# Kernel optimization log

Hardware: AMD Instinct MI355X
Metric: run time of the kernel (lower is better)

The kernel has to match this reference:

```python
import jax, jax.numpy as jnp
import numpy as np

HIDDEN = 2048
NH = 32        # query heads
NKV = 4        # kv heads
D = 128        # head dim
T = 2048       # tokens
WINDOW = 512   # sliding window
EPS = 1e-6
THETA = 1000000.0
SCALE = D ** -0.5


def setup_inputs() -> dict:
    key = jax.random.key(0)
    k1, k2, k3 = jax.random.split(key, 3)
    return {
        "positions": jnp.arange(T, dtype=jnp.int64) if jax.config.jax_enable_x64 else jnp.arange(T, dtype=jnp.int32),
        "hidden_states": jax.random.normal(k1, (T, HIDDEN), dtype=jnp.float32),
        "w_qkv": jax.random.normal(k2, (HIDDEN, (NH + 2 * NKV) * D), dtype=jnp.float32) * 0.02,
        "w_o": jax.random.normal(k3, (NH * D, HIDDEN), dtype=jnp.float32) * 0.02,
        "q_norm_w": jnp.ones((D,), dtype=jnp.float32),
        "k_norm_w": jnp.ones((D,), dtype=jnp.float32),
    }


def _rms_norm(x, w):
    # x: [..., D]; per-head RMSNorm
    var = jnp.mean(x * x, axis=-1, keepdims=True)
    return x * jax.lax.rsqrt(var + EPS) * w


def _rope(x, positions):
    # x: [T, H, D], neox-style rotary over full head dim
    inv_freq = 1.0 / (THETA ** (jnp.arange(0, D, 2, dtype=jnp.float32) / D))  # [D/2]
    freqs = positions.astype(jnp.float32)[:, None] * inv_freq                 # [T, D/2]
    cos = jnp.cos(freqs)[:, None, :]
    sin = jnp.sin(freqs)[:, None, :]
    x1, x2 = x[..., : D // 2], x[..., D // 2 :]
    return jnp.concatenate([x1 * cos - x2 * sin, x2 * cos + x1 * sin], axis=-1)


def reference(positions, hidden_states, w_qkv, w_o, q_norm_w, k_norm_w):
    qkv = hidden_states @ w_qkv                                   # [T, (NH+2NKV)*D]
    q, k, v = jnp.split(qkv, [NH * D, (NH + NKV) * D], axis=-1)
    q = _rms_norm(q.reshape(T, NH, D), q_norm_w)
    k = _rms_norm(k.reshape(T, NKV, D), k_norm_w)
    v = v.reshape(T, NKV, D)
    q = _rope(q, positions)
    k = _rope(k, positions)
    # GQA: expand kv heads to query heads
    rep = NH // NKV
    k = jnp.repeat(k, rep, axis=1)                                # [T, NH, D]
    v = jnp.repeat(v, rep, axis=1)
    scores = jnp.einsum("qhd,khd->hqk", q, k) * SCALE             # [NH, T, T]
    i = jnp.arange(T)[:, None]
    j = jnp.arange(T)[None, :]
    mask = (j <= i) & (i - j < WINDOW)                            # causal sliding window
    scores = jnp.where(mask[None, :, :], scores, jnp.finfo(scores.dtype).min)
    probs = jax.nn.softmax(scores, axis=-1)
    out = jnp.einsum("hqk,khd->qhd", probs, v).reshape(T, NH * D)
    return out @ w_o
```

## Files before the change

### kernel.cpp

```cpp
#include <hip/hip_runtime.h>
#include <math.h>

#define T      2048
#define HIDDEN 2048
#define NH     32
#define NKV    4
#define D      128
#define WINDOW 512
#define QKVW   ((NH + 2 * NKV) * D)
#define ODIM   (NH * D)
#define EPS    1e-6f
#define SCALE  0.08838834764831845f
#define PSTR   68
#define ESTR   136
#define VSTR   36
#define QMUL   ((float)(0.08838834764831845 * 1.4426950408889634))
#define MLOG2E 5.7707801635558536f

typedef _Float16 f16x8 __attribute__((ext_vector_type(8)));
typedef _Float16 f16x4 __attribute__((ext_vector_type(4)));
typedef float    f32x4 __attribute__((ext_vector_type(4)));


__device__ __forceinline__ void gl2lds16(const void* g, void* l) {
  __builtin_amdgcn_global_load_lds((const __attribute__((address_space(1))) void*)g,
                                   (__attribute__((address_space(3))) void*)l,
                                   16, 0, 0);
}

#define NB_A  2048
#define NB_B1 2560
#define NB_B2 2048

__device__ __forceinline__ void pack_b_region(const float* __restrict__ W,
                                              _Float16* __restrict__ Bp,
                                              int N, int kt, int ng, int tid,
                                              _Float16* __restrict__ LS) {
  const int r = tid >> 3;
  const int c0 = (tid & 7) * 16;
  const float* src = W + (size_t)(kt * 32 + r) * N + ng * 128 + c0;
#pragma unroll
  for (int v = 0; v < 4; ++v) {
    const float4 f = *(const float4*)(src + v * 4);
    LS[r * 132 + c0 + v * 4 + 0] = (_Float16)f.x;
    LS[r * 132 + c0 + v * 4 + 1] = (_Float16)f.y;
    LS[r * 132 + c0 + v * 4 + 2] = (_Float16)f.z;
    LS[r * 132 + c0 + v * 4 + 3] = (_Float16)f.w;
  }
  __syncthreads();
#pragma unroll
  for (int i = 0; i < 2; ++i) {
    const int ch = tid * 2 + i;
    const int tile = ch >> 6;
    const int cc = ch & 63;
    const int q = cc >> 4, o = cc & 15;
    f16x8 v;
#pragma unroll
    for (int j = 0; j < 8; ++j) v[j] = LS[(q * 8 + j) * 132 + tile * 16 + o];
    *(f16x8*)(Bp + ((size_t)(kt * (N / 16) + ng * 8 + tile) * 512) + cc * 8) = v;
  }
}

__global__ __launch_bounds__(256)
void prep(const float* __restrict__ hidden, const float* __restrict__ w_qkv,
          const float* __restrict__ w_o, const int* __restrict__ positions,
          _Float16* __restrict__ Ah1, _Float16* __restrict__ Bp1,
          _Float16* __restrict__ Bp2, float* __restrict__ cosT,
          float* __restrict__ sinT) {
  __shared__ _Float16 LS[32 * 132];
  const int bx = blockIdx.x;
  const int tid = threadIdx.x;
  if (bx < NB_A) {
    const int cid = bx * 256 + tid;
    const int c = cid & 63;
    const int tile = cid >> 6;
    const int mtg = tile & (T / 16 - 1);
    const int kt = tile >> 7;
    const float* src = hidden + (size_t)(mtg * 16 + (c & 15)) * HIDDEN + kt * 32 + (c >> 4) * 8;
    const float4 a = *(const float4*)src;
    const float4 b = *(const float4*)(src + 4);
    f16x8 h;
    h[0] = (_Float16)a.x; h[1] = (_Float16)a.y; h[2] = (_Float16)a.z; h[3] = (_Float16)a.w;
    h[4] = (_Float16)b.x; h[5] = (_Float16)b.y; h[6] = (_Float16)b.z; h[7] = (_Float16)b.w;
    *(f16x8*)(Ah1 + (size_t)cid * 8) = h;
  } else if (bx < NB_A + NB_B1) {
    const int idx = bx - NB_A;
    pack_b_region(w_qkv, Bp1, QKVW, idx / 40, idx % 40, tid, LS);
  } else if (bx < NB_A + NB_B1 + NB_B2) {
    const int idx = bx - NB_A - NB_B1;
    pack_b_region(w_o, Bp2, HIDDEN, idx / 16, idx % 16, tid, LS);
  } else {
    const int p0 = (bx - NB_A - NB_B1 - NB_B2) * 64 + (tid >> 6) * 16;
    const int j = tid & 63;
    const float invf = (float)pow(1.0e6, -(double)j / 64.0);
#pragma unroll 4
    for (int i = 0; i < 16; ++i) {
      const int t = p0 + i;
      const float ang = (float)positions[t] * invf;
      cosT[t * 64 + j] = cosf(ang);
      sinT[t * 64 + j] = sinf(ang);
    }
  }
}

#define KSTEPS 64

__global__ __launch_bounds__(256, 3)
void gemm_qkv(const _Float16* __restrict__ Apk, const _Float16* __restrict__ Bpk,
              const float* __restrict__ qnw, const float* __restrict__ knw,
              const float* __restrict__ cosT, const float* __restrict__ sinT,
              _Float16* __restrict__ Qpk, _Float16* __restrict__ Kpk,
              _Float16* __restrict__ Vpk) {
  extern __shared__ _Float16 SM[];
  const int tid = threadIdx.x;
  const int lane = tid & 63;
  const int wv = tid >> 6;
  const int l15 = lane & 15;
  const int l4 = lane >> 4;
  const int bx = blockIdx.x, by = blockIdx.y;

  f32x4 acc[2][8];
#pragma unroll
  for (int i = 0; i < 2; ++i)
#pragma unroll
    for (int j = 0; j < 8; ++j) acc[i][j] = (f32x4)0.f;

  auto stage = [&](int k, int s) {
    const int u = wv * 4 + s;
    char* dst = (char*)SM + (k % 3) * 16384 +
                (u < 8 ? u * 1024 : 8192 + (u - 8) * 1024);
    const char* src = (u < 8)
        ? (const char*)Apk + ((size_t)k * (T / 16) + by * 8 + u) * 1024 + lane * 16
        : (const char*)Bpk + ((size_t)k * (QKVW / 16) + bx * 8 + (u - 8)) * 1024 + lane * 16;
    gl2lds16(src, dst);
  };

#pragma unroll
  for (int k = 0; k < 2; ++k)
#pragma unroll
    for (int s = 0; s < 4; ++s) stage(k, s);
  asm volatile("s_waitcnt vmcnt(4)" ::: "memory");
  __builtin_amdgcn_s_barrier();
  __builtin_amdgcn_sched_barrier(0);

  int slot = 0;
  for (int t = 0; t < KSTEPS; ++t) {
    const _Float16* As = SM + slot * 8192;
    const _Float16* Bs = As + 4096;
    f16x8 af[2], bf[8];
#pragma unroll
    for (int i = 0; i < 2; ++i)
      af[i] = *(const f16x8*)(As + (wv * 2 + i) * 512 + lane * 8);
#pragma unroll
    for (int j = 0; j < 8; ++j)
      bf[j] = *(const f16x8*)(Bs + j * 512 + lane * 8);
    if (t + 2 < KSTEPS)
#pragma unroll
      for (int s = 0; s < 4; ++s) stage(t + 2, s);
    __builtin_amdgcn_s_setprio(1);
#pragma unroll
    for (int i = 0; i < 2; ++i)
#pragma unroll
      for (int j = 0; j < 8; ++j)
        acc[i][j] = __builtin_amdgcn_mfma_f32_16x16x32_f16(af[i], bf[j], acc[i][j], 0, 0, 0);
    __builtin_amdgcn_s_setprio(0);
    if (t < KSTEPS - 2)       asm volatile("s_waitcnt vmcnt(4)" ::: "memory");
    else if (t == KSTEPS - 2) asm volatile("s_waitcnt vmcnt(0)" ::: "memory");
    __builtin_amdgcn_s_barrier();
    __builtin_amdgcn_sched_barrier(0);
    slot = (slot == 2) ? 0 : slot + 1;
  }
  __syncthreads();

  if (bx < NH + NKV) {
    const bool isq = bx < NH;
    const float* w = isq ? qnw : knw;
    const float omul = isq ? QMUL : 1.0f;
    float wcol[8];
#pragma unroll
    for (int j = 0; j < 8; ++j) wcol[j] = w[j * 16 + l15];

    _Float16* ex = SM + wv * (32 * ESTR);
#pragma unroll
    for (int i = 0; i < 2; ++i)
#pragma unroll
      for (int r = 0; r < 4; ++r) {
        float ss = 0.f;
#pragma unroll
        for (int j = 0; j < 8; ++j) ss += acc[i][j][r] * acc[i][j][r];
        ss += __shfl_xor(ss, 1); ss += __shfl_xor(ss, 2);
        ss += __shfl_xor(ss, 4); ss += __shfl_xor(ss, 8);
        const float rn = 1.0f / sqrtf(ss * (1.0f / D) + EPS);
        const int row = i * 16 + l4 * 4 + r;
        const int t = by * 128 + wv * 32 + row;
#pragma unroll
        for (int j = 0; j < 4; ++j) {
          const int jc = j * 16 + l15;
          const float c = cosT[t * 64 + jc];
          const float s = sinT[t * 64 + jc];
          const float x1 = acc[i][j][r] * rn * wcol[j];
          const float x2 = acc[i][j + 4][r] * rn * wcol[j + 4];
          ex[row * ESTR + jc]      = (_Float16)((x1 * c - x2 * s) * omul);
          ex[row * ESTR + 64 + jc] = (_Float16)((x2 * c + x1 * s) * omul);
        }
      }
    const int hl = isq ? bx : bx - NH;
    _Float16* dst0 = isq ? Qpk : Kpk;
#pragma unroll
    for (int u = 0; u < 2; ++u) {
      const int qt = by * 8 + wv * 2 + u;
#pragma unroll
      for (int ds = 0; ds < 4; ++ds) {
        const f16x8 frag = *(const f16x8*)(ex + (u * 16 + l15) * ESTR + ds * 32 + l4 * 8);
        *(f16x8*)(dst0 + ((size_t)(hl * 128 + qt) * 4 + ds) * 512 + lane * 8) = frag;
      }
    }
  } else {
    const int kvh = bx - NH - NKV;
    _Float16* exv = SM + wv * (128 * VSTR);
#pragma unroll
    for (int i = 0; i < 2; ++i)
#pragma unroll
      for (int j = 0; j < 8; ++j) {
        f16x4 v4;
#pragma unroll
        for (int r = 0; r < 4; ++r) v4[r] = (_Float16)acc[i][j][r];
        *(f16x4*)(exv + (j * 16 + l15) * VSTR + i * 16 + l4 * 4) = v4;
      }
    const int kt64 = by * 2 + (wv >> 1);
    const int ks = wv & 1;
#pragma unroll
    for (int dt = 0; dt < 8; ++dt) {
      const f16x4 lo = *(const f16x4*)(exv + (dt * 16 + l15) * VSTR + l4 * 8);
      const f16x4 hi = *(const f16x4*)(exv + (dt * 16 + l15) * VSTR + l4 * 8 + 4);
      f16x8 h8;
#pragma unroll
      for (int r = 0; r < 4; ++r) { h8[r] = lo[r]; h8[r + 4] = hi[r]; }
      *(f16x8*)(Vpk + (((size_t)(kvh * 32 + kt64) * 2 + ks) * 8 + dt) * 512 + lane * 8) = h8;
    }
  }
}

__global__ __launch_bounds__(256, 3)
void gemm_f16p(const _Float16* __restrict__ Apk, const _Float16* __restrict__ Bpk,
               float* __restrict__ C0, float* __restrict__ C1,
               int M, int N, int nkt) {
  extern __shared__ _Float16 SM[];
  const int tid = threadIdx.x;
  const int lane = tid & 63;
  const int wv = tid >> 6;
  const int wr = wv & 1, wc = wv >> 1;
  const int kt0 = blockIdx.z * nkt;
  float* __restrict__ C = blockIdx.z ? C1 : C0;

  f32x4 acc[4][4];
#pragma unroll
  for (int i = 0; i < 4; ++i)
#pragma unroll
    for (int j = 0; j < 4; ++j) acc[i][j] = (f32x4)0.f;

  const size_t Astep = (size_t)(M >> 4) * 1024;
  const size_t Bstep = (size_t)(N >> 4) * 1024;
  const char* Ag = (const char*)Apk + (size_t)kt0 * Astep +
                   (size_t)(blockIdx.y * 8) * 1024 + lane * 16;
  const char* Bg = (const char*)Bpk + (size_t)kt0 * Bstep +
                   (size_t)(blockIdx.x * 8) * 1024 + lane * 16;

  auto stage = [&](int k, int s) {
    const int u = wv * 4 + s;
    char* dst = (char*)SM + (k % 3) * 16384 +
                (u < 8 ? u * 1024 : 8192 + (u - 8) * 1024);
    const char* src = (u < 8) ? Ag + (size_t)k * Astep + u * 1024
                              : Bg + (size_t)k * Bstep + (u - 8) * 1024;
    gl2lds16(src, dst);
  };

#pragma unroll
  for (int k = 0; k < 2; ++k)
#pragma unroll
    for (int s = 0; s < 4; ++s) stage(k, s);
  asm volatile("s_waitcnt vmcnt(4)" ::: "memory");
  __builtin_amdgcn_s_barrier();
  __builtin_amdgcn_sched_barrier(0);

  int slot = 0;
  for (int t = 0; t < nkt; ++t) {
    const _Float16* As = SM + slot * 8192;
    const _Float16* Bs = As + 4096;
    f16x8 af[4], bf[4];
#pragma unroll
    for (int i = 0; i < 4; ++i)
      af[i] = *(const f16x8*)(As + (wr * 4 + i) * 512 + lane * 8);
#pragma unroll
    for (int j = 0; j < 4; ++j)
      bf[j] = *(const f16x8*)(Bs + (wc * 4 + j) * 512 + lane * 8);
    if (t + 2 < nkt)
#pragma unroll
      for (int s = 0; s < 4; ++s) stage(t + 2, s);
    __builtin_amdgcn_s_setprio(1);
#pragma unroll
    for (int i = 0; i < 4; ++i)
#pragma unroll
      for (int j = 0; j < 4; ++j)
        acc[i][j] = __builtin_amdgcn_mfma_f32_16x16x32_f16(af[i], bf[j], acc[i][j], 0, 0, 0);
    __builtin_amdgcn_s_setprio(0);
    if (t < nkt - 2)       asm volatile("s_waitcnt vmcnt(4)" ::: "memory");
    else if (t == nkt - 2) asm volatile("s_waitcnt vmcnt(0)" ::: "memory");
    __builtin_amdgcn_s_barrier();
    __builtin_amdgcn_sched_barrier(0);
    slot = (slot == 2) ? 0 : slot + 1;
  }

  const int row0 = blockIdx.y * 128 + wr * 64 + ((lane >> 4) << 2);
  const int col0 = blockIdx.x * 128 + wc * 64 + (lane & 15);
#pragma unroll
  for (int i = 0; i < 4; ++i)
#pragma unroll
    for (int j = 0; j < 4; ++j) {
#pragma unroll
      for (int r = 0; r < 4; ++r)
        C[(size_t)(row0 + i * 16 + r) * N + col0 + j * 16] = acc[i][j][r];
    }
}

__global__ __launch_bounds__(256)
void reduce_add(const float4* __restrict__ a, const float4* __restrict__ b,
                float4* __restrict__ o, int n4) {
  for (int i = blockIdx.x * 256 + threadIdx.x; i < n4; i += gridDim.x * 256) {
    const float4 x = a[i], y = b[i];
    o[i] = make_float4(x.x + y.x, x.y + y.y, x.z + y.z, x.w + y.w);
  }
}

__global__ __launch_bounds__(256)
void attn_mfma(const _Float16* __restrict__ Qpk, const _Float16* __restrict__ Kpk,
               const _Float16* __restrict__ Vpk, _Float16* __restrict__ Ap2) {
  const int h = blockIdx.x;
  const int q0 = blockIdx.y * 128;
  const int kvh = h >> 3;
  const int tid = threadIdx.x;
  const int lane = tid & 63;
  const int wv = tid >> 6;
  const int l15 = lane & 15;
  const int l4 = lane >> 4;

  __shared__ _Float16 SM[8192 + 2 * 8192 + 4 * 32 * PSTR];
  _Float16* Ks = SM;
  _Float16* Vs = SM + 8192;
  _Float16* Pw = SM + 24576 + wv * 32 * PSTR;

  f16x8 qfA[4], qfB[4];
  {
    const _Float16* qa = Qpk + ((size_t)h * 128 + (q0 >> 4) + wv * 2) * 2048 + lane * 8;
#pragma unroll
    for (int ds = 0; ds < 4; ++ds) {
      qfA[ds] = *(const f16x8*)(qa + ds * 512);
      qfB[ds] = *(const f16x8*)(qa + 2048 + ds * 512);
    }
  }

  f16x8 ones;
#pragma unroll
  for (int j = 0; j < 8; ++j) ones[j] = (_Float16)1.0f;

  f32x4 OA[8], OB[8];
#pragma unroll
  for (int dt = 0; dt < 8; ++dt) { OA[dt] = (f32x4)0.f; OB[dt] = (f32x4)0.f; }
  f32x4 LA = (f32x4)0.f, LB = (f32x4)0.f;

  int kstart = q0 - (WINDOW - 1);
  if (kstart < 0) kstart = 0;
  kstart &= ~63;
  const int kend = q0 + 128;

  auto stageKV = [&](int kt2, int vb) {
    const _Float16* Kg = Kpk + ((size_t)kvh * 128 + (kt2 >> 4)) * 2048 + lane * 8;
    const _Float16* Vg = Vpk + ((size_t)kvh * 32 + (kt2 >> 6)) * 8192 + lane * 8;
#pragma unroll
    for (int t = wv; t < 16; t += 4) {
      gl2lds16(Kg + t * 512, (char*)Ks + t * 1024);
      gl2lds16(Vg + t * 512, (char*)(Vs + vb * 8192) + t * 1024);
    }
  };

  stageKV(kstart, 0);
  asm volatile("s_waitcnt vmcnt(0)" ::: "memory");
  __builtin_amdgcn_s_barrier();
  __builtin_amdgcn_sched_barrier(0);

  int vbuf = 0;
  for (int kt = kstart; kt < kend; kt += 64) {
    f32x4 sA[4], sB[4];
#pragma unroll
    for (int nt = 0; nt < 4; ++nt) { sA[nt] = (f32x4)(-MLOG2E); sB[nt] = (f32x4)(-MLOG2E); }
    __builtin_amdgcn_s_setprio(1);
#pragma unroll
    for (int ds = 0; ds < 4; ++ds) {
#pragma unroll
      for (int nt = 0; nt < 4; ++nt) {
        const f16x8 kf = *(const f16x8*)(Ks + (nt * 4 + ds) * 512 + lane * 8);
        sA[nt] = __builtin_amdgcn_mfma_f32_16x16x32_f16(qfA[ds], kf, sA[nt], 0, 0, 0);
        sB[nt] = __builtin_amdgcn_mfma_f32_16x16x32_f16(qfB[ds], kf, sB[nt], 0, 0, 0);
      }
    }
    __builtin_amdgcn_s_setprio(0);
    __builtin_amdgcn_s_barrier();
    __builtin_amdgcn_sched_barrier(0);
    if (kt + 64 < kend) stageKV(kt + 64, vbuf ^ 1);

    const int qbA = q0 + wv * 32 + l4 * 4;
    const int kb = kt + l15;
#pragma unroll
    for (int nt = 0; nt < 4; ++nt) {
      const int kidx = kb + nt * 16;
#pragma unroll
      for (int r = 0; r < 4; ++r) {
        float pA = __builtin_amdgcn_exp2f(sA[nt][r]);
        float pB = __builtin_amdgcn_exp2f(sB[nt][r]);
        pA = ((unsigned)(qbA + r - kidx) < WINDOW) ? pA : 0.f;
        pB = ((unsigned)(qbA + 16 + r - kidx) < WINDOW) ? pB : 0.f;
        Pw[(l4 * 4 + r) * PSTR + nt * 16 + l15] = (_Float16)pA;
        Pw[(16 + l4 * 4 + r) * PSTR + nt * 16 + l15] = (_Float16)pB;
      }
    }

    const _Float16* Vcur = Vs + vbuf * 8192;
    __builtin_amdgcn_s_setprio(1);
#pragma unroll
    for (int ks = 0; ks < 2; ++ks) {
      const f16x8 pfA = *(const f16x8*)(Pw + l15 * PSTR + ks * 32 + l4 * 8);
      const f16x8 pfB = *(const f16x8*)(Pw + (16 + l15) * PSTR + ks * 32 + l4 * 8);
      LA = __builtin_amdgcn_mfma_f32_16x16x32_f16(pfA, ones, LA, 0, 0, 0);
      LB = __builtin_amdgcn_mfma_f32_16x16x32_f16(pfB, ones, LB, 0, 0, 0);
#pragma unroll
      for (int dt = 0; dt < 8; ++dt) {
        const f16x8 vf = *(const f16x8*)(Vcur + (ks * 8 + dt) * 512 + lane * 8);
        OA[dt] = __builtin_amdgcn_mfma_f32_16x16x32_f16(pfA, vf, OA[dt], 0, 0, 0);
        OB[dt] = __builtin_amdgcn_mfma_f32_16x16x32_f16(pfB, vf, OB[dt], 0, 0, 0);
      }
    }
    __builtin_amdgcn_s_setprio(0);
    asm volatile("s_waitcnt vmcnt(0)" ::: "memory");
    __builtin_amdgcn_s_barrier();
    __builtin_amdgcn_sched_barrier(0);
    vbuf ^= 1;
  }

  _Float16* Tw = SM + wv * 16 * ESTR;
#pragma unroll
  for (int half = 0; half < 2; ++half) {
    const f32x4* O = half ? OB : OA;
    const f32x4  L = half ? LB : LA;
    float inv[4];
#pragma unroll
    for (int r = 0; r < 4; ++r) inv[r] = 1.0f / L[r];
#pragma unroll
    for (int dt = 0; dt < 8; ++dt)
#pragma unroll
      for (int r = 0; r < 4; ++r)
        Tw[(l4 * 4 + r) * ESTR + dt * 16 + l15] = (_Float16)(O[dt][r] * inv[r]);
    const int qt = (q0 >> 4) + wv * 2 + half;
#pragma unroll
    for (int ds = 0; ds < 4; ++ds) {
      const f16x8 frag = *(const f16x8*)(Tw + l15 * ESTR + ds * 32 + l4 * 8);
      *(f16x8*)(Ap2 + ((size_t)(h * 4 + ds) * 128 + qt) * 512 + lane * 8) = frag;
    }
  }
}

extern "C" void kernel_launch(void* const* d_in, const int* in_sizes, int n_in,
                              void* d_out, int out_size, void* d_ws, size_t ws_size,
                              hipStream_t stream) {
  const int*   positions = (const int*)d_in[0];
  const float* hidden    = (const float*)d_in[1];
  const float* w_qkv     = (const float*)d_in[2];
  const float* w_o       = (const float*)d_in[3];
  const float* q_norm_w  = (const float*)d_in[4];
  const float* k_norm_w  = (const float*)d_in[5];
  float* out = (float*)d_out;

  char* ws = (char*)d_ws;
  _Float16* Kpk = (_Float16*)ws;
  _Float16* Vpk = Kpk + (size_t)T * NKV * D;
  ws += (size_t)T * QKVW * 4;
  _Float16* Ap2 = (_Float16*)ws;
  float* P0 = (float*)(ws + (size_t)T * ODIM * 2);
  ws += (size_t)T * ODIM * 4;
  float* cosT = (float*)ws;  ws += (size_t)T * 64 * 4;
  float* sinT = (float*)ws;  ws += (size_t)T * 64 * 4;
  _Float16* Bp1 = (_Float16*)ws; ws += (size_t)HIDDEN * QKVW * 2;
  _Float16* Bp2 = (_Float16*)ws; ws += (size_t)ODIM * HIDDEN * 2;
  _Float16* Ah1 = (_Float16*)ws; ws += (size_t)T * HIDDEN * 2;
  _Float16* Qpk = (_Float16*)ws;
  float* P1 = (float*)Qpk;
  ws += (size_t)T * ODIM * 2;

  prep<<<dim3(NB_A + NB_B1 + NB_B2 + T / 64), 256, 0, stream>>>(
      hidden, w_qkv, w_o, positions, Ah1, Bp1, Bp2, cosT, sinT);

  gemm_qkv<<<dim3(QKVW / 128, T / 128), 256, 49152, stream>>>(
      Ah1, Bp1, q_norm_w, k_norm_w, cosT, sinT, Qpk, Kpk, Vpk);

  attn_mfma<<<dim3(NH, T / 128), 256, 0, stream>>>(Qpk, Kpk, Vpk, Ap2);

  gemm_f16p<<<dim3(HIDDEN / 128, T / 128, 2), 256, 49152, stream>>>(
      Ap2, Bp2, P0, P1, T, HIDDEN, ODIM / 32 / 2);
  reduce_add<<<dim3(1024), 256, 0, stream>>>((const float4*)P0, (const float4*)P1,
                                             (float4*)out, T * HIDDEN / 4);
}
```

Measured before the change: 268.8 us.

## Split QKV GEMM tile across eight waves instead of four

The QKV projection kernel now runs with 512 threads per block. Each wave computes one 16-row slab of the 128x128 tile instead of two, and the global-to-LDS staging is spread over twice as many waves. The epilogue for norm/RoPE and V packing is re-indexed to match, with an added block barrier in the V path. The aim is more waves per CU to hide latency and fewer accumulator registers per thread, at the cost of each wave reusing its B fragments over fewer MFMAs (more LDS reads per MFMA).

```diff
diff --git a/kernel.cpp b/kernel.cpp
--- a/kernel.cpp
+++ b/kernel.cpp
@@ -105,7 +105,7 @@
 
 #define KSTEPS 64
 
-__global__ __launch_bounds__(256, 3)
+__global__ __launch_bounds__(512, 6)
 void gemm_qkv(const _Float16* __restrict__ Apk, const _Float16* __restrict__ Bpk,
               const float* __restrict__ qnw, const float* __restrict__ knw,
               const float* __restrict__ cosT, const float* __restrict__ sinT,
@@ -119,14 +119,12 @@
   const int l4 = lane >> 4;
   const int bx = blockIdx.x, by = blockIdx.y;
 
-  f32x4 acc[2][8];
-#pragma unroll
-  for (int i = 0; i < 2; ++i)
-#pragma unroll
-    for (int j = 0; j < 8; ++j) acc[i][j] = (f32x4)0.f;
+  f32x4 acc[8];
+#pragma unroll
+  for (int j = 0; j < 8; ++j) acc[j] = (f32x4)0.f;
 
   auto stage = [&](int k, int s) {
-    const int u = wv * 4 + s;
+    const int u = wv * 2 + s;
     char* dst = (char*)SM + (k % 3) * 16384 +
                 (u < 8 ? u * 1024 : 8192 + (u - 8) * 1024);
     const char* src = (u < 8)
@@ -138,8 +136,8 @@
 #pragma unroll
   for (int k = 0; k < 2; ++k)
 #pragma unroll
-    for (int s = 0; s < 4; ++s) stage(k, s);
-  asm volatile("s_waitcnt vmcnt(4)" ::: "memory");
+    for (int s = 0; s < 2; ++s) stage(k, s);
+  asm volatile("s_waitcnt vmcnt(2)" ::: "memory");
   __builtin_amdgcn_s_barrier();
   __builtin_amdgcn_sched_barrier(0);
 
@@ -147,24 +145,18 @@
   for (int t = 0; t < KSTEPS; ++t) {
     const _Float16* As = SM + slot * 8192;
     const _Float16* Bs = As + 4096;
-    f16x8 af[2], bf[8];
-#pragma unroll
-    for (int i = 0; i < 2; ++i)
-      af[i] = *(const f16x8*)(As + (wv * 2 + i) * 512 + lane * 8);
+    f16x8 af, bf[8];
+    af = *(const f16x8*)(As + wv * 512 + lane * 8);
 #pragma unroll
     for (int j = 0; j < 8; ++j)
       bf[j] = *(const f16x8*)(Bs + j * 512 + lane * 8);
-    if (t + 2 < KSTEPS)
-#pragma unroll
-      for (int s = 0; s < 4; ++s) stage(t + 2, s);
+    if (t + 2 < KSTEPS) { stage(t + 2, 0); stage(t + 2, 1); }
     __builtin_amdgcn_s_setprio(1);
 #pragma unroll
-    for (int i = 0; i < 2; ++i)
-#pragma unroll
-      for (int j = 0; j < 8; ++j)
-        acc[i][j] = __builtin_amdgcn_mfma_f32_16x16x32_f16(af[i], bf[j], acc[i][j], 0, 0, 0);
+    for (int j = 0; j < 8; ++j)
+      acc[j] = __builtin_amdgcn_mfma_f32_16x16x32_f16(af, bf[j], acc[j], 0, 0, 0);
     __builtin_amdgcn_s_setprio(0);
-    if (t < KSTEPS - 2)       asm volatile("s_waitcnt vmcnt(4)" ::: "memory");
+    if (t < KSTEPS - 2)       asm volatile("s_waitcnt vmcnt(2)" ::: "memory");
     else if (t == KSTEPS - 2) asm volatile("s_waitcnt vmcnt(0)" ::: "memory");
     __builtin_amdgcn_s_barrier();
     __builtin_amdgcn_sched_barrier(0);
@@ -180,57 +172,52 @@
 #pragma unroll
     for (int j = 0; j < 8; ++j) wcol[j] = w[j * 16 + l15];
 
-    _Float16* ex = SM + wv * (32 * ESTR);
-#pragma unroll
-    for (int i = 0; i < 2; ++i)
-#pragma unroll
-      for (int r = 0; r < 4; ++r) {
-        float ss = 0.f;
-#pragma unroll
-        for (int j = 0; j < 8; ++j) ss += acc[i][j][r] * acc[i][j][r];
-        ss += __shfl_xor(ss, 1); ss += __shfl_xor(ss, 2);
-        ss += __shfl_xor(ss, 4); ss += __shfl_xor(ss, 8);
-        const float rn = 1.0f / sqrtf(ss * (1.0f / D) + EPS);
-        const int row = i * 16 + l4 * 4 + r;
-        const int t = by * 128 + wv * 32 + row;
-#pragma unroll
-        for (int j = 0; j < 4; ++j) {
-          const int jc = j * 16 + l15;
-          const float c = cosT[t * 64 + jc];
-          const float s = sinT[t * 64 + jc];
-          const float x1 = acc[i][j][r] * rn * wcol[j];
-          const float x2 = acc[i][j + 4][r] * rn * wcol[j + 4];
-          ex[row * ESTR + jc]      = (_Float16)((x1 * c - x2 * s) * omul);
-          ex[row * ESTR + 64 + jc] = (_Float16)((x2 * c + x1 * s) * omul);
-        }
+    _Float16* ex = SM + wv * (16 * ESTR);
+#pragma unroll
+    for (int r = 0; r < 4; ++r) {
+      float ss = 0.f;
+#pragma unroll
+      for (int j = 0; j < 8; ++j) ss += acc[j][r] * acc[j][r];
+      ss += __shfl_xor(ss, 1); ss += __shfl_xor(ss, 2);
+      ss += __shfl_xor(ss, 4); ss += __shfl_xor(ss, 8);
+      const float rn = 1.0f / sqrtf(ss * (1.0f / D) + EPS);
+      const int row = l4 * 4 + r;
+      const int tok = by * 128 + wv * 16 + row;
+#pragma unroll
+      for (int j = 0; j < 4; ++j) {
+        const int jc = j * 16 + l15;
+        const float c = cosT[tok * 64 + jc];
+        const float s = sinT[tok * 64 + jc];
+        const float x1 = acc[j][r] * rn * wcol[j];
+        const float x2 = acc[j + 4][r] * rn * wcol[j + 4];
+        ex[row * ESTR + jc]      = (_Float16)((x1 * c - x2 * s) * omul);
+        ex[row * ESTR + 64 + jc] = (_Float16)((x2 * c + x1 * s) * omul);
       }
+    }
     const int hl = isq ? bx : bx - NH;
     _Float16* dst0 = isq ? Qpk : Kpk;
-#pragma unroll
-    for (int u = 0; u < 2; ++u) {
-      const int qt = by * 8 + wv * 2 + u;
-#pragma unroll
-      for (int ds = 0; ds < 4; ++ds) {
-        const f16x8 frag = *(const f16x8*)(ex + (u * 16 + l15) * ESTR + ds * 32 + l4 * 8);
-        *(f16x8*)(dst0 + ((size_t)(hl * 128 + qt) * 4 + ds) * 512 + lane * 8) = frag;
-      }
+    const int qt = by * 8 + wv;
+#pragma unroll
+    for (int ds = 0; ds < 4; ++ds) {
+      const f16x8 frag = *(const f16x8*)(ex + l15 * ESTR + ds * 32 + l4 * 8);
+      *(f16x8*)(dst0 + ((size_t)(hl * 128 + qt) * 4 + ds) * 512 + lane * 8) = frag;
     }
   } else {
     const int kvh = bx - NH - NKV;
-    _Float16* exv = SM + wv * (128 * VSTR);
-#pragma unroll
-    for (int i = 0; i < 2; ++i)
-#pragma unroll
-      for (int j = 0; j < 8; ++j) {
-        f16x4 v4;
-#pragma unroll
-        for (int r = 0; r < 4; ++r) v4[r] = (_Float16)acc[i][j][r];
-        *(f16x4*)(exv + (j * 16 + l15) * VSTR + i * 16 + l4 * 4) = v4;
-      }
-    const int kt64 = by * 2 + (wv >> 1);
-    const int ks = wv & 1;
-#pragma unroll
-    for (int dt = 0; dt < 8; ++dt) {
+    _Float16* exv = SM + (wv >> 1) * (128 * VSTR);
+#pragma unroll
+    for (int j = 0; j < 8; ++j) {
+      f16x4 v4;
+#pragma unroll
+      for (int r = 0; r < 4; ++r) v4[r] = (_Float16)acc[j][r];
+      *(f16x4*)(exv + (j * 16 + l15) * VSTR + (wv & 1) * 16 + l4 * 4) = v4;
+    }
+    __syncthreads();
+    const int kt64 = by * 2 + (wv >> 2);
+    const int ks = (wv >> 1) & 1;
+#pragma unroll
+    for (int dtt = 0; dtt < 4; ++dtt) {
+      const int dt = (wv & 1) * 4 + dtt;
       const f16x4 lo = *(const f16x4*)(exv + (dt * 16 + l15) * VSTR + l4 * 8);
       const f16x4 hi = *(const f16x4*)(exv + (dt * 16 + l15) * VSTR + l4 * 8 + 4);
       f16x8 h8;
@@ -498,7 +485,7 @@
   prep<<<dim3(NB_A + NB_B1 + NB_B2 + T / 64), 256, 0, stream>>>(
       hidden, w_qkv, w_o, positions, Ah1, Bp1, Bp2, cosT, sinT);
 
-  gemm_qkv<<<dim3(QKVW / 128, T / 128), 256, 49152, stream>>>(
+  gemm_qkv<<<dim3(QKVW / 128, T / 128), 512, 49152, stream>>>(
       Ah1, Bp1, q_norm_w, k_norm_w, cosT, sinT, Qpk, Kpk, Vpk);
 
   attn_mfma<<<dim3(NH, T / 128), 256, 0, stream>>>(Qpk, Kpk, Vpk, Ap2);
```

Result: slower. 303.6 us (+12.9%).
